# Performance work log

Measured on AMD Instinct MI355X. Metric: run time of the kernel, lower is better.

Reference implementation:

```python
import jax, jax.numpy as jnp
import numpy as np

NODE_DIM = 64
OUT_DIM = 64
EDGE_DIM = 64
N_NODES = 50000
N_EDGES = 800000
BN_EPS = 1e-5


def _batchnorm(x, gamma, beta):
    # training-mode BatchNorm1d: biased batch statistics
    mean = jnp.mean(x, axis=0)
    var = jnp.mean((x - mean) ** 2, axis=0)
    return (x - mean) * jax.lax.rsqrt(var + BN_EPS) * gamma + beta


def setup_inputs() -> dict:
    key = jax.random.key(0)
    ks = jax.random.split(key, 16)
    s = 0.05  # weight init scale
    inp = {
        "em": jax.random.normal(ks[0], (N_NODES, NODE_DIM), jnp.float32),
        "edge_index": jax.random.randint(ks[1], (2, N_EDGES), 0, N_NODES, jnp.int64),
        "edge_features": jax.random.normal(ks[2], (N_EDGES, EDGE_DIM), jnp.float32),
        # GINEConv edge linear (edge_dim -> node_dim)
        "W_le": jax.random.normal(ks[3], (EDGE_DIM, NODE_DIM), jnp.float32) * s,
        "b_le": jnp.zeros((NODE_DIM,), jnp.float32),
        # GINEConv nn: Linear(node_dim, out) -> ReLU -> Linear(out, out)
        "W1": jax.random.normal(ks[4], (NODE_DIM, OUT_DIM), jnp.float32) * s,
        "b1": jnp.zeros((OUT_DIM,), jnp.float32),
        "W2": jax.random.normal(ks[5], (OUT_DIM, OUT_DIM), jnp.float32) * s,
        "b2": jnp.zeros((OUT_DIM,), jnp.float32),
        # x BatchNorm affine
        "gx": jnp.ones((OUT_DIM,), jnp.float32),
        "bx": jnp.zeros((OUT_DIM,), jnp.float32),
        # edge MLP: (edge_dim + 2*out) -> out -> out -> out
        "We1": jax.random.normal(ks[6], (EDGE_DIM + 2 * OUT_DIM, OUT_DIM), jnp.float32) * s,
        "be1": jnp.zeros((OUT_DIM,), jnp.float32),
        "We2": jax.random.normal(ks[7], (OUT_DIM, OUT_DIM), jnp.float32) * s,
        "be2": jnp.zeros((OUT_DIM,), jnp.float32),
        "We3": jax.random.normal(ks[8], (OUT_DIM, OUT_DIM), jnp.float32) * s,
        "be3": jnp.zeros((OUT_DIM,), jnp.float32),
        # edge BatchNorm affine
        "ge": jnp.ones((OUT_DIM,), jnp.float32),
        "be": jnp.zeros((OUT_DIM,), jnp.float32),
    }
    return inp


def reference(em, edge_index, edge_features, W_le, b_le, W1, b1, W2, b2, gx, bx,
              We1, be1, We2, be2, We3, be3, ge, be):
    src, dst = edge_index[0], edge_index[1]
    # GINEConv: msg = relu(x_j + lin(edge_attr)), sum-aggregated at target
    msg = jax.nn.relu(em[src] + edge_features @ W_le + b_le)  # [E, node_dim]
    aggr = jax.ops.segment_sum(msg, dst, num_segments=em.shape[0])  # [N, node_dim]
    h = em + aggr  # eps = 0
    h = jax.nn.relu(h @ W1 + b1) @ W2 + b2  # [N, out]
    x_em = jax.nn.relu(_batchnorm(h, gx, bx))
    # edge update: concat(x_em[src], x_em[dst], edge_features)
    edge_mess = jnp.concatenate([x_em[src], x_em[dst], edge_features], axis=1)
    e = jax.nn.relu(edge_mess @ We1 + be1)
    e = jax.nn.relu(e @ We2 + be2)
    e = e @ We3 + be3
    edge_out = jax.nn.relu(_batchnorm(e, ge, be))
    return x_em, edge_out
```

## Files before the change

### kernel.cpp

```cpp
#include <hip/hip_runtime.h>
#include <cstddef>
#include <cstdint>

#define NN 50000
#define NE 800000

typedef __bf16 bf16x8 __attribute__((ext_vector_type(8)));
typedef float  f32x4  __attribute__((ext_vector_type(4)));

__device__ __forceinline__ bf16x8 ldfrag(const __bf16* __restrict__ wfr, int f, int lane) {
    return *reinterpret_cast<const bf16x8*>(wfr + (size_t)(f * 64 + lane) * 8);
}
__device__ __forceinline__ f32x4 mfma16(bf16x8 a, bf16x8 b, f32x4 c) {
    return __builtin_amdgcn_mfma_f32_16x16x32_bf16(a, b, c, 0, 0, 0);
}
__device__ __forceinline__ bool idx_is64(const int* eidx) {
    return ((eidx[1] | eidx[3] | eidx[5] | eidx[7]) == 0);
}
__device__ __forceinline__ int ld_src(const int* eidx, bool is64, int e) {
    return is64 ? eidx[(size_t)2 * e] : eidx[e];
}
__device__ __forceinline__ int ld_dst(const int* eidx, bool is64, int e) {
    return is64 ? eidx[2 * ((size_t)NE + e)] : eidx[(size_t)NE + e];
}
__device__ __forceinline__ bf16x8 cvt8(const float* __restrict__ p) {
    float4 v0 = *reinterpret_cast<const float4*>(p);
    float4 v1 = *reinterpret_cast<const float4*>(p + 4);
    bf16x8 r;
    r[0] = (__bf16)v0.x; r[1] = (__bf16)v0.y; r[2] = (__bf16)v0.z; r[3] = (__bf16)v0.w;
    r[4] = (__bf16)v1.x; r[5] = (__bf16)v1.y; r[6] = (__bf16)v1.z; r[7] = (__bf16)v1.w;
    return r;
}

__global__ __launch_bounds__(256) void prep(const float* __restrict__ wle, const float* __restrict__ w1,
                                            const float* __restrict__ w2, const float* __restrict__ we1,
                                            const float* __restrict__ we2, const float* __restrict__ we3,
                                            __bf16* __restrict__ wfr) {
    int sid = blockIdx.x * 256 + threadIdx.x;
    int f = sid >> 6, lane = sid & 63;
    const float* W; int fo;
    if (f < 8)       { W = wle; fo = 0; }
    else if (f < 16) { W = w1;  fo = 8; }
    else if (f < 24) { W = w2;  fo = 16; }
    else if (f < 48) { W = we1; fo = 24; }
    else if (f < 56) { W = we2; fo = 48; }
    else             { W = we3; fo = 56; }
    int lf = f - fo, kt = lf >> 2, nt = lf & 3;
    int g = lane >> 4, c = lane & 15;
#pragma unroll
    for (int b = 0; b < 8; b++) {
        int k = kt * 32 + g * 8 + b;
        int n = nt * 16 + c;
        wfr[(size_t)(f * 64 + lane) * 8 + b] = (__bf16)W[(size_t)k * 64 + n];
    }
}

__global__ __launch_bounds__(256) void k1(const float* __restrict__ em, const int* __restrict__ eidx,
                                          const float* __restrict__ ef, const __bf16* __restrict__ wfr,
                                          const float* __restrict__ ble, float* __restrict__ nodebuf) {
    __shared__ __bf16 Ash[64][72];
    const int t = threadIdx.x;
    const int base = blockIdx.x * 64;
    {
        const int r = t >> 2, seg = t & 3;
        const float4* p = reinterpret_cast<const float4*>(ef + (size_t)(base + r) * 64 + seg * 16);
#pragma unroll
        for (int i = 0; i < 4; i++) {
            float4 v = p[i];
            int cb = seg * 16 + i * 4;
            Ash[r][cb + 0] = (__bf16)v.x; Ash[r][cb + 1] = (__bf16)v.y;
            Ash[r][cb + 2] = (__bf16)v.z; Ash[r][cb + 3] = (__bf16)v.w;
        }
    }
    const bool is64 = idx_is64(eidx);
    __syncthreads();
    const int lane = t & 63, w = t >> 6, c = lane & 15, g = lane >> 4;
    const int arow = w * 16 + c;
    f32x4 acc[4] = {{0.f,0.f,0.f,0.f},{0.f,0.f,0.f,0.f},{0.f,0.f,0.f,0.f},{0.f,0.f,0.f,0.f}};
#pragma unroll
    for (int kt = 0; kt < 2; kt++) {
        bf16x8 a = *reinterpret_cast<const bf16x8*>(&Ash[arow][kt * 32 + g * 8]);
#pragma unroll
        for (int nt = 0; nt < 4; nt++) acc[nt] = mfma16(a, ldfrag(wfr, kt * 4 + nt, lane), acc[nt]);
    }
#pragma unroll
    for (int rr = 0; rr < 4; rr++) {
        int e = base + w * 16 + g * 4 + rr;
        int sn = ld_src(eidx, is64, e);
        int dn = ld_dst(eidx, is64, e);
#pragma unroll
        for (int nt = 0; nt < 4; nt++) {
            int col = nt * 16 + c;
            float v = acc[nt][rr] + ble[col] + em[(size_t)sn * 64 + col];
            if (v > 0.f) atomicAdd(&nodebuf[(size_t)dn * 64 + col], v);
        }
    }
}

__global__ __launch_bounds__(256) void k2(const float* __restrict__ em, float* __restrict__ nb,
                                          const __bf16* __restrict__ wfr, const float* __restrict__ b1,
                                          const float* __restrict__ b2, float* __restrict__ sums) {
    __shared__ __bf16 Ysh[64][72];
    __shared__ float bs[128];
    const int t = threadIdx.x;
    const int base = blockIdx.x * 64;
    if (t < 128) bs[t] = 0.f;
    __syncthreads();
    const int lane = t & 63, w = t >> 6, c = lane & 15, g = lane >> 4;
    const int arow = base + w * 16 + c;
    const size_t rl = (size_t)(arow < NN ? arow : NN - 1) * 64;
    bf16x8 a[2];
#pragma unroll
    for (int kt = 0; kt < 2; kt++) {
        int off = kt * 32 + g * 8;
        float4 e0 = *reinterpret_cast<const float4*>(em + rl + off);
        float4 e1 = *reinterpret_cast<const float4*>(em + rl + off + 4);
        float4 n0 = *reinterpret_cast<const float4*>(nb + rl + off);
        float4 n1 = *reinterpret_cast<const float4*>(nb + rl + off + 4);
        bf16x8 r;
        r[0] = (__bf16)(e0.x + n0.x); r[1] = (__bf16)(e0.y + n0.y);
        r[2] = (__bf16)(e0.z + n0.z); r[3] = (__bf16)(e0.w + n0.w);
        r[4] = (__bf16)(e1.x + n1.x); r[5] = (__bf16)(e1.y + n1.y);
        r[6] = (__bf16)(e1.z + n1.z); r[7] = (__bf16)(e1.w + n1.w);
        a[kt] = r;
    }
    f32x4 a1[4] = {{0.f,0.f,0.f,0.f},{0.f,0.f,0.f,0.f},{0.f,0.f,0.f,0.f},{0.f,0.f,0.f,0.f}};
#pragma unroll
    for (int kt = 0; kt < 2; kt++)
#pragma unroll
        for (int nt = 0; nt < 4; nt++) a1[nt] = mfma16(a[kt], ldfrag(wfr, 8 + kt * 4 + nt, lane), a1[nt]);
#pragma unroll
    for (int nt = 0; nt < 4; nt++) {
        float bb = b1[nt * 16 + c];
#pragma unroll
        for (int rr = 0; rr < 4; rr++) {
            float v = a1[nt][rr] + bb;
            v = v > 0.f ? v : 0.f;
            Ysh[w * 16 + g * 4 + rr][nt * 16 + c] = (__bf16)v;
        }
    }
    bf16x8 ya[2];
#pragma unroll
    for (int kt = 0; kt < 2; kt++)
        ya[kt] = *reinterpret_cast<const bf16x8*>(&Ysh[w * 16 + c][kt * 32 + g * 8]);
    f32x4 a2[4] = {{0.f,0.f,0.f,0.f},{0.f,0.f,0.f,0.f},{0.f,0.f,0.f,0.f},{0.f,0.f,0.f,0.f}};
#pragma unroll
    for (int kt = 0; kt < 2; kt++)
#pragma unroll
        for (int nt = 0; nt < 4; nt++) a2[nt] = mfma16(ya[kt], ldfrag(wfr, 16 + kt * 4 + nt, lane), a2[nt]);
#pragma unroll
    for (int nt = 0; nt < 4; nt++) {
        int col = nt * 16 + c;
        float bb = b2[col];
        float ss = 0.f, qq = 0.f;
#pragma unroll
        for (int rr = 0; rr < 4; rr++) {
            int row = base + w * 16 + g * 4 + rr;
            if (row < NN) {
                float v = a2[nt][rr] + bb;
                nb[(size_t)row * 64 + col] = v;
                ss += v; qq += v * v;
            }
        }
        ss += __shfl_xor(ss, 16); ss += __shfl_xor(ss, 32);
        qq += __shfl_xor(qq, 16); qq += __shfl_xor(qq, 32);
        if (g == 0) { atomicAdd(&bs[col], ss); atomicAdd(&bs[64 + col], qq); }
    }
    __syncthreads();
    if (t < 128) atomicAdd(&sums[t], bs[t]);
}

__global__ __launch_bounds__(256) void k3(float* __restrict__ nb, const float* __restrict__ sums,
                                          const float* __restrict__ gx, const float* __restrict__ bx,
                                          __bf16* __restrict__ wsx) {
    size_t i4 = (size_t)(blockIdx.x * 256 + threadIdx.x) * 4;
    int col0 = (int)(i4 & 63);
    float4 v = *reinterpret_cast<const float4*>(nb + i4);
    const float* pv = reinterpret_cast<const float*>(&v);
    float o[4]; short so[4];
#pragma unroll
    for (int j = 0; j < 4; j++) {
        int col = col0 + j;
        float m   = sums[col] * (1.0f / 50000.0f);
        float var = sums[64 + col] * (1.0f / 50000.0f) - m * m;
        float inv = rsqrtf(var + 1e-5f);
        float x = (pv[j] - m) * inv * gx[col] + bx[col];
        x = x > 0.f ? x : 0.f;
        o[j] = x;
        so[j] = __builtin_bit_cast(short, (__bf16)x);
    }
    *reinterpret_cast<float4*>(nb + i4) = make_float4(o[0], o[1], o[2], o[3]);
    *reinterpret_cast<short4*>(wsx + i4) = make_short4(so[0], so[1], so[2], so[3]);
}

__global__ __launch_bounds__(256) void k4(const int* __restrict__ eidx, const float* __restrict__ ef,
                                          const __bf16* __restrict__ wsx, const __bf16* __restrict__ wfr,
                                          const float* __restrict__ be1, const float* __restrict__ be2,
                                          const float* __restrict__ be3, float* __restrict__ eout,
                                          float* __restrict__ pws) {
    __shared__ __bf16 Ysh[2][64][72];
    __shared__ float bs[128];
    const int t = threadIdx.x;
    const int blockb = blockIdx.x * 128;
    if (t < 128) bs[t] = 0.f;
    __syncthreads();
    const int lane = t & 63, w = t >> 6, c = lane & 15, g = lane >> 4;
    const bool is64 = idx_is64(eidx);

    int erow[2], sn[2], dn[2];
    bf16x8 xs[2][2], xd[2][2], ea[2][2];
#pragma unroll
    for (int tt = 0; tt < 2; tt++) {
        erow[tt] = blockb + tt * 64 + w * 16 + c;
        sn[tt] = ld_src(eidx, is64, erow[tt]);
        dn[tt] = ld_dst(eidx, is64, erow[tt]);
#pragma unroll
        for (int kt = 0; kt < 2; kt++) {
            int off = kt * 32 + g * 8;
            xs[tt][kt] = *reinterpret_cast<const bf16x8*>(wsx + (size_t)sn[tt] * 64 + off);
            xd[tt][kt] = *reinterpret_cast<const bf16x8*>(wsx + (size_t)dn[tt] * 64 + off);
            ea[tt][kt] = cvt8(ef + (size_t)erow[tt] * 64 + off);
        }
    }
    f32x4 a1[2][4];
#pragma unroll
    for (int tt = 0; tt < 2; tt++)
#pragma unroll
        for (int nt = 0; nt < 4; nt++) a1[tt][nt] = f32x4{0.f,0.f,0.f,0.f};
#pragma unroll
    for (int tt = 0; tt < 2; tt++)
#pragma unroll
        for (int kt = 0; kt < 2; kt++)
#pragma unroll
            for (int nt = 0; nt < 4; nt++) a1[tt][nt] = mfma16(xs[tt][kt], ldfrag(wfr, 24 + kt * 4 + nt, lane), a1[tt][nt]);
#pragma unroll
    for (int tt = 0; tt < 2; tt++)
#pragma unroll
        for (int kt = 0; kt < 2; kt++)
#pragma unroll
            for (int nt = 0; nt < 4; nt++) a1[tt][nt] = mfma16(xd[tt][kt], ldfrag(wfr, 32 + kt * 4 + nt, lane), a1[tt][nt]);
#pragma unroll
    for (int tt = 0; tt < 2; tt++)
#pragma unroll
        for (int kt = 0; kt < 2; kt++)
#pragma unroll
            for (int nt = 0; nt < 4; nt++) a1[tt][nt] = mfma16(ea[tt][kt], ldfrag(wfr, 40 + kt * 4 + nt, lane), a1[tt][nt]);
#pragma unroll
    for (int tt = 0; tt < 2; tt++)
#pragma unroll
        for (int nt = 0; nt < 4; nt++) {
            float bb = be1[nt * 16 + c];
#pragma unroll
            for (int rr = 0; rr < 4; rr++) {
                float v = a1[tt][nt][rr] + bb;
                v = v > 0.f ? v : 0.f;
                Ysh[tt][w * 16 + g * 4 + rr][nt * 16 + c] = (__bf16)v;
            }
        }
    bf16x8 ya[2][2];
#pragma unroll
    for (int tt = 0; tt < 2; tt++)
#pragma unroll
        for (int kt = 0; kt < 2; kt++)
            ya[tt][kt] = *reinterpret_cast<const bf16x8*>(&Ysh[tt][w * 16 + c][kt * 32 + g * 8]);
    f32x4 a2[2][4];
#pragma unroll
    for (int tt = 0; tt < 2; tt++)
#pragma unroll
        for (int nt = 0; nt < 4; nt++) a2[tt][nt] = f32x4{0.f,0.f,0.f,0.f};
#pragma unroll
    for (int tt = 0; tt < 2; tt++)
#pragma unroll
        for (int kt = 0; kt < 2; kt++)
#pragma unroll
            for (int nt = 0; nt < 4; nt++) a2[tt][nt] = mfma16(ya[tt][kt], ldfrag(wfr, 48 + kt * 4 + nt, lane), a2[tt][nt]);
#pragma unroll
    for (int tt = 0; tt < 2; tt++)
#pragma unroll
        for (int nt = 0; nt < 4; nt++) {
            float bb = be2[nt * 16 + c];
#pragma unroll
            for (int rr = 0; rr < 4; rr++) {
                float v = a2[tt][nt][rr] + bb;
                v = v > 0.f ? v : 0.f;
                Ysh[tt][w * 16 + g * 4 + rr][nt * 16 + c] = (__bf16)v;
            }
        }
#pragma unroll
    for (int tt = 0; tt < 2; tt++)
#pragma unroll
        for (int kt = 0; kt < 2; kt++)
            ya[tt][kt] = *reinterpret_cast<const bf16x8*>(&Ysh[tt][w * 16 + c][kt * 32 + g * 8]);
    f32x4 a3[2][4];
#pragma unroll
    for (int tt = 0; tt < 2; tt++)
#pragma unroll
        for (int nt = 0; nt < 4; nt++) a3[tt][nt] = f32x4{0.f,0.f,0.f,0.f};
#pragma unroll
    for (int tt = 0; tt < 2; tt++)
#pragma unroll
        for (int kt = 0; kt < 2; kt++)
#pragma unroll
            for (int nt = 0; nt < 4; nt++) a3[tt][nt] = mfma16(ya[tt][kt], ldfrag(wfr, 56 + kt * 4 + nt, lane), a3[tt][nt]);
#pragma unroll
    for (int tt = 0; tt < 2; tt++)
#pragma unroll
        for (int nt = 0; nt < 4; nt++) {
            int col = nt * 16 + c;
            float bb = be3[col];
            float ss = 0.f, qq = 0.f;
#pragma unroll
            for (int rr = 0; rr < 4; rr++) {
                int e = blockb + tt * 64 + w * 16 + g * 4 + rr;
                float v = a3[tt][nt][rr] + bb;
                eout[(size_t)e * 64 + col] = v;
                ss += v; qq += v * v;
            }
            ss += __shfl_xor(ss, 16); ss += __shfl_xor(ss, 32);
            qq += __shfl_xor(qq, 16); qq += __shfl_xor(qq, 32);
            if (g == 0) { atomicAdd(&bs[col], ss); atomicAdd(&bs[64 + col], qq); }
        }
    __syncthreads();
    if (t < 128) pws[(size_t)t * (NE / 128) + blockIdx.x] = bs[t];
}

__global__ __launch_bounds__(256) void k4r(const float* __restrict__ pws, float* __restrict__ sums) {
    int b = blockIdx.x;
    float s = 0.f;
    for (int i = threadIdx.x; i < NE / 128; i += 256) s += pws[(size_t)b * (NE / 128) + i];
#pragma unroll
    for (int m = 32; m >= 1; m >>= 1) s += __shfl_xor(s, m);
    __shared__ float acc4[4];
    int lane = threadIdx.x & 63, wid = threadIdx.x >> 6;
    if (lane == 0) acc4[wid] = s;
    __syncthreads();
    if (threadIdx.x == 0) sums[128 + b] = acc4[0] + acc4[1] + acc4[2] + acc4[3];
}

__global__ __launch_bounds__(256) void k5(float* __restrict__ eo, const float* __restrict__ sums,
                                          const float* __restrict__ ge, const float* __restrict__ be) {
    size_t i4 = (size_t)(blockIdx.x * 256 + threadIdx.x) * 4;
    int col0 = (int)(i4 & 63);
    float4 v = *reinterpret_cast<const float4*>(eo + i4);
    const float* pv = reinterpret_cast<const float*>(&v);
    float o[4];
#pragma unroll
    for (int j = 0; j < 4; j++) {
        int col = col0 + j;
        float m   = sums[128 + col] * (1.0f / 800000.0f);
        float var = sums[192 + col] * (1.0f / 800000.0f) - m * m;
        float inv = rsqrtf(var + 1e-5f);
        float x = (pv[j] - m) * inv * ge[col] + be[col];
        o[j] = x > 0.f ? x : 0.f;
    }
    *reinterpret_cast<float4*>(eo + i4) = make_float4(o[0], o[1], o[2], o[3]);
}

extern "C" void kernel_launch(void* const* d_in, const int* in_sizes, int n_in,
                              void* d_out, int out_size, void* d_ws, size_t ws_size,
                              hipStream_t stream) {
    const float* em   = (const float*)d_in[0];
    const int*   eidx = (const int*)d_in[1];
    const float* ef   = (const float*)d_in[2];
    const float* b_le = (const float*)d_in[4];
    const float* b1   = (const float*)d_in[6];
    const float* b2   = (const float*)d_in[8];
    const float* gx   = (const float*)d_in[9];
    const float* bx   = (const float*)d_in[10];
    const float* be1  = (const float*)d_in[12];
    const float* be2  = (const float*)d_in[14];
    const float* be3  = (const float*)d_in[16];
    const float* ge   = (const float*)d_in[17];
    const float* be   = (const float*)d_in[18];

    float* out = (float*)d_out;
    float* nodebuf = out;
    float* eout = out + (size_t)NN * 64;

    float*  sums = (float*)d_ws;
    __bf16* wfr  = (__bf16*)((char*)d_ws + 1024);
    __bf16* wsx  = (__bf16*)((char*)d_ws + 1024 + 65536);
    float*  pws  = (float*)((char*)d_ws + 1024 + 65536 + (size_t)NN * 64 * 2);

    hipMemsetAsync(sums, 0, 256 * sizeof(float), stream);
    hipMemsetAsync(nodebuf, 0, (size_t)NN * 64 * sizeof(float), stream);

    prep<<<16, 256, 0, stream>>>((const float*)d_in[3], (const float*)d_in[5], (const float*)d_in[7],
                                 (const float*)d_in[11], (const float*)d_in[13], (const float*)d_in[15], wfr);
    k1<<<NE / 64, 256, 0, stream>>>(em, eidx, ef, wfr, b_le, nodebuf);
    k2<<<(NN + 63) / 64, 256, 0, stream>>>(em, nodebuf, wfr, b1, b2, sums);
    k3<<<(NN * 64) / 1024, 256, 0, stream>>>(nodebuf, sums, gx, bx, wsx);
    k4<<<NE / 128, 256, 0, stream>>>(eidx, ef, wsx, wfr, be1, be2, be3, eout, pws);
    k4r<<<128, 256, 0, stream>>>(pws, sums);
    k5<<<((size_t)NE * 64) / 1024, 256, 0, stream>>>(eout, sums, ge, be);
}
```

Before: 473.7 us.

## Sort edges by destination via CSR before message scatter

Adds degree count, a single-block prefix scan and a fill kernel that build a destination-sorted edge permutation, then processes edges in that order in the message kernel. Edges hitting the same destination row land in the same wave or block, so atomic adds should get better locality and less contention. In exchange it adds three kernels, including a serial one-block scan, plus extra atomics for counting and filling. Edge features are now gathered in permuted order rather than read contiguously.

```diff
diff --git a/kernel.cpp b/kernel.cpp
--- a/kernel.cpp
+++ b/kernel.cpp
@@ -55,44 +55,74 @@
     }
 }
 
-__global__ __launch_bounds__(256) void k1(const float* __restrict__ em, const int* __restrict__ eidx,
-                                          const float* __restrict__ ef, const __bf16* __restrict__ wfr,
-                                          const float* __restrict__ ble, float* __restrict__ nodebuf) {
-    __shared__ __bf16 Ash[64][72];
+__global__ __launch_bounds__(256) void kdeg(const int* __restrict__ eidx, int* __restrict__ cnt) {
+    const bool is64 = idx_is64(eidx);
+    int e = blockIdx.x * 256 + threadIdx.x;
+    atomicAdd(&cnt[ld_dst(eidx, is64, e)], 1);
+}
+
+__global__ __launch_bounds__(1024) void kscan(const int* __restrict__ cnt, int* __restrict__ rowptr) {
+    __shared__ int ps[1024];
+    const int t = threadIdx.x;
+    const int CH = (NN + 1023) / 1024;
+    const int b0 = t * CH;
+    int s = 0;
+    for (int i = 0; i < CH; i++) { int n = b0 + i; if (n < NN) s += cnt[n]; }
+    ps[t] = s;
+    __syncthreads();
+    for (int off = 1; off < 1024; off <<= 1) {
+        int v = (t >= off) ? ps[t - off] : 0;
+        __syncthreads();
+        ps[t] += v;
+        __syncthreads();
+    }
+    int run = (t == 0) ? 0 : ps[t - 1];
+    for (int i = 0; i < CH; i++) {
+        int n = b0 + i;
+        if (n < NN) { rowptr[n] = run; run += cnt[n]; }
+    }
+    if (t == 1023) rowptr[NN] = ps[1023];
+}
+
+__global__ __launch_bounds__(256) void kfill(const int* __restrict__ eidx, int* __restrict__ cnt2,
+                                             const int* __restrict__ rowptr, int* __restrict__ eid) {
+    const bool is64 = idx_is64(eidx);
+    int e = blockIdx.x * 256 + threadIdx.x;
+    int dn = ld_dst(eidx, is64, e);
+    int slot = rowptr[dn] + atomicAdd(&cnt2[dn], 1);
+    eid[slot] = e;
+}
+
+__global__ __launch_bounds__(256) void k1p(const float* __restrict__ em, const int* __restrict__ eidx,
+                                           const float* __restrict__ ef, const __bf16* __restrict__ wfr,
+                                           const float* __restrict__ ble, const int* __restrict__ eid,
+                                           float* __restrict__ nodebuf) {
     const int t = threadIdx.x;
     const int base = blockIdx.x * 64;
-    {
-        const int r = t >> 2, seg = t & 3;
-        const float4* p = reinterpret_cast<const float4*>(ef + (size_t)(base + r) * 64 + seg * 16);
-#pragma unroll
-        for (int i = 0; i < 4; i++) {
-            float4 v = p[i];
-            int cb = seg * 16 + i * 4;
-            Ash[r][cb + 0] = (__bf16)v.x; Ash[r][cb + 1] = (__bf16)v.y;
-            Ash[r][cb + 2] = (__bf16)v.z; Ash[r][cb + 3] = (__bf16)v.w;
-        }
-    }
+    const int lane = t & 63, w = t >> 6, c = lane & 15, g = lane >> 4;
     const bool is64 = idx_is64(eidx);
-    __syncthreads();
-    const int lane = t & 63, w = t >> 6, c = lane & 15, g = lane >> 4;
-    const int arow = w * 16 + c;
+    const int ea_e = eid[base + w * 16 + c];
+    bf16x8 a[2];
+#pragma unroll
+    for (int kt = 0; kt < 2; kt++)
+        a[kt] = cvt8(ef + (size_t)ea_e * 64 + kt * 32 + g * 8);
     f32x4 acc[4] = {{0.f,0.f,0.f,0.f},{0.f,0.f,0.f,0.f},{0.f,0.f,0.f,0.f},{0.f,0.f,0.f,0.f}};
 #pragma unroll
-    for (int kt = 0; kt < 2; kt++) {
-        bf16x8 a = *reinterpret_cast<const bf16x8*>(&Ash[arow][kt * 32 + g * 8]);
-#pragma unroll
-        for (int nt = 0; nt < 4; nt++) acc[nt] = mfma16(a, ldfrag(wfr, kt * 4 + nt, lane), acc[nt]);
-    }
+    for (int kt = 0; kt < 2; kt++)
+#pragma unroll
+        for (int nt = 0; nt < 4; nt++) acc[nt] = mfma16(a[kt], ldfrag(wfr, kt * 4 + nt, lane), acc[nt]);
 #pragma unroll
     for (int rr = 0; rr < 4; rr++) {
-        int e = base + w * 16 + g * 4 + rr;
+        int pos = base + w * 16 + g * 4 + rr;
+        int e = eid[pos];
         int sn = ld_src(eidx, is64, e);
         int dn = ld_dst(eidx, is64, e);
+        float* nrow = nodebuf + (size_t)dn * 64;
 #pragma unroll
         for (int nt = 0; nt < 4; nt++) {
             int col = nt * 16 + c;
             float v = acc[nt][rr] + ble[col] + em[(size_t)sn * 64 + col];
-            if (v > 0.f) atomicAdd(&nodebuf[(size_t)dn * 64 + col], v);
+            if (v > 0.f) atomicAdd(nrow + col, v);
         }
     }
 }
@@ -377,17 +407,27 @@
     float* nodebuf = out;
     float* eout = out + (size_t)NN * 64;
 
-    float*  sums = (float*)d_ws;
-    __bf16* wfr  = (__bf16*)((char*)d_ws + 1024);
-    __bf16* wsx  = (__bf16*)((char*)d_ws + 1024 + 65536);
-    float*  pws  = (float*)((char*)d_ws + 1024 + 65536 + (size_t)NN * 64 * 2);
+    char* wsb = (char*)d_ws;
+    float*  sums   = (float*)wsb;
+    __bf16* wfr    = (__bf16*)(wsb + 1024);
+    __bf16* wsx    = (__bf16*)(wsb + 1024 + 65536);
+    size_t  off    = 1024 + 65536 + (size_t)NN * 64 * 2;
+    float*  pws    = (float*)(wsb + off);          off += (size_t)128 * (NE / 128) * 4;
+    int*    cnt    = (int*)(wsb + off);            off += 200192;
+    int*    cnt2   = (int*)(wsb + off);            off += 200192;
+    int*    rowptr = (int*)(wsb + off);            off += 200192;
+    int*    eid    = (int*)(wsb + off);
 
     hipMemsetAsync(sums, 0, 256 * sizeof(float), stream);
     hipMemsetAsync(nodebuf, 0, (size_t)NN * 64 * sizeof(float), stream);
+    hipMemsetAsync(cnt, 0, 200192 * 2, stream);
 
     prep<<<16, 256, 0, stream>>>((const float*)d_in[3], (const float*)d_in[5], (const float*)d_in[7],
                                  (const float*)d_in[11], (const float*)d_in[13], (const float*)d_in[15], wfr);
-    k1<<<NE / 64, 256, 0, stream>>>(em, eidx, ef, wfr, b_le, nodebuf);
+    kdeg<<<NE / 256, 256, 0, stream>>>(eidx, cnt);
+    kscan<<<1, 1024, 0, stream>>>(cnt, rowptr);
+    kfill<<<NE / 256, 256, 0, stream>>>(eidx, cnt2, rowptr, eid);
+    k1p<<<NE / 64, 256, 0, stream>>>(em, eidx, ef, wfr, b_le, eid, nodebuf);
     k2<<<(NN + 63) / 64, 256, 0, stream>>>(em, nodebuf, wfr, b1, b2, sums);
     k3<<<(NN * 64) / 1024, 256, 0, stream>>>(nodebuf, sums, gx, bx, wsx);
     k4<<<NE / 128, 256, 0, stream>>>(eidx, ef, wsx, wfr, be1, be2, be3, eout, pws);
```

Measured after the change: 826.7 us. +74.5%, slower.
